# Optimization experiments

Measured on AMD Instinct MI355X. Metric: run time of the kernel, lower is better.

The kernel has to match this reference:

```python
import jax, jax.numpy as jnp
import numpy as np

NUM_HEADS = 16
HIDDEN = 1024
HEADSIZE = HIDDEN // NUM_HEADS


def setup_inputs() -> dict:
    key = jax.random.key(0)
    ks = jax.random.split(key, 9)
    B, S, H = 4, 2048, HIDDEN
    s = 1.0 / np.sqrt(H)
    return {
        "x": jax.random.normal(ks[0], (B, S, H), dtype=jnp.float32),
        "Wq": jax.random.normal(ks[1], (H, H), dtype=jnp.float32) * s,
        "bq": jax.random.normal(ks[2], (H,), dtype=jnp.float32) * s,
        "Wk": jax.random.normal(ks[3], (H, H), dtype=jnp.float32) * s,
        "bk": jax.random.normal(ks[4], (H,), dtype=jnp.float32) * s,
        "Wv": jax.random.normal(ks[5], (H, H), dtype=jnp.float32) * s,
        "bv": jax.random.normal(ks[6], (H,), dtype=jnp.float32) * s,
        "Wo": jax.random.normal(ks[7], (H, H), dtype=jnp.float32) * s,
        "bo": jax.random.normal(ks[8], (H,), dtype=jnp.float32) * s,
    }


def reference(x, Wq, bq, Wk, bk, Wv, bv, Wo, bo):
    B, S, H = x.shape
    nh, hs = NUM_HEADS, HEADSIZE

    def split_heads(y):  # (B,S,H) -> (B,nh,S,hs)
        return y.reshape(B, S, nh, hs).transpose(0, 2, 1, 3)

    q = split_heads(x @ Wq.T + bq)
    k = split_heads(x @ Wk.T + bk)
    v = split_heads(x @ Wv.T + bv)

    scores = jnp.einsum("bhqd,bhkd->bhqk", q, k) / jnp.sqrt(jnp.float32(hs))
    # causal mask: q_ind < k_ind gets -1e9 (matches torch.where(mask, -1e9, scores))
    q_ind = jnp.arange(S)[:, None]
    k_ind = jnp.arange(S)[None, :]
    scores = jnp.where(q_ind < k_ind, jnp.float32(-1e9), scores)
    attn = jax.nn.softmax(scores, axis=-1)
    out = jnp.einsum("bhqk,bhkd->bhqd", attn, v)  # (B,nh,S,hs)
    out = out.transpose(0, 2, 1, 3).reshape(B, S, H)
    return out @ Wo.T + bo
```

## Files before the change

### kernel.cpp

```cpp
#include <hip/hip_runtime.h>

#define NH 16
#define HS 64
#define HID 1024
#define SEQ 2048
#define BB 4
#define MR (BB*SEQ)
#define KD 1024
#define QSCALE 0.18033688f

typedef __bf16 bf16;
typedef __attribute__((ext_vector_type(8))) __bf16 bf16x8;
typedef __attribute__((ext_vector_type(4))) __bf16 bf16x4;
typedef __attribute__((ext_vector_type(4))) float f32x4;
typedef __attribute__((ext_vector_type(16))) float f32x16;
typedef __attribute__((ext_vector_type(4))) float f4;
typedef __attribute__((ext_vector_type(2))) unsigned uintx2;

typedef __attribute__((address_space(3))) unsigned int as3u;
typedef __attribute__((address_space(1))) unsigned int as1u;

__device__ __forceinline__ void gl_lds16(const void* g, void* l) {
  __builtin_amdgcn_global_load_lds((const as1u*)g, (as3u*)l, 16, 0, 0);
}

__device__ __forceinline__ f32x4 mfma16(bf16x8 a, bf16x8 b, f32x4 c) {
  return __builtin_amdgcn_mfma_f32_16x16x32_bf16(a, b, c, 0, 0, 0);
}

__device__ __forceinline__ f32x16 mfma32(bf16x8 a, bf16x8 b, f32x16 c) {
  return __builtin_amdgcn_mfma_f32_32x32x16_bf16(a, b, c, 0, 0, 0);
}

__device__ __forceinline__ uintx2 plswap(unsigned a, unsigned b) {
#if __has_builtin(__builtin_amdgcn_permlane32_swap)
  return __builtin_amdgcn_permlane32_swap(a, b, false, false);
#else
  asm volatile("v_permlane32_swap_b32 %0, %1" : "+&v"(a), "+v"(b));
  uintx2 r; r[0] = a; r[1] = b; return r;
#endif
}

__device__ __forceinline__ float xmax32(float x) {
  uintx2 r = plswap(__float_as_uint(x), __float_as_uint(x));
  return fmaxf(__uint_as_float(r[0]), __uint_as_float(r[1]));
}
__device__ __forceinline__ float xadd32(float x) {
  uintx2 r = plswap(__float_as_uint(x), __float_as_uint(x));
  return __uint_as_float(r[0]) + __uint_as_float(r[1]);
}

__device__ __forceinline__ unsigned cvtpk(float lo, float hi) {
  unsigned r;
  asm("v_cvt_pk_bf16_f32 %0, %1, %2" : "=v"(r) : "v"(lo), "v"(hi));
  return r;
}

__global__ __launch_bounds__(256) void k_cvt(const float* __restrict__ in,
                                             bf16* __restrict__ out, int n4) {
  int i = blockIdx.x * 256 + threadIdx.x;
  if (i >= n4) return;
  f4 v = reinterpret_cast<const f4*>(in)[i];
  bf16x4 h;
  h[0] = (bf16)v[0]; h[1] = (bf16)v[1]; h[2] = (bf16)v[2]; h[3] = (bf16)v[3];
  reinterpret_cast<bf16x4*>(out)[i] = h;
}

__global__ __launch_bounds__(256) void k_cvt4(const float* __restrict__ w0, const float* __restrict__ w1,
                                              const float* __restrict__ w2, const float* __restrict__ w3,
                                              bf16* __restrict__ o0, bf16* __restrict__ o1,
                                              bf16* __restrict__ o2, bf16* __restrict__ o3, int n4) {
  int i = blockIdx.x * 256 + threadIdx.x;
  if (i >= n4) return;
  const float* in = (blockIdx.y == 0) ? w0 : (blockIdx.y == 1) ? w1 : (blockIdx.y == 2) ? w2 : w3;
  bf16* out = (blockIdx.y == 0) ? o0 : (blockIdx.y == 1) ? o1 : (blockIdx.y == 2) ? o2 : o3;
  f4 v = reinterpret_cast<const f4*>(in)[i];
  bf16x4 h;
  h[0] = (bf16)v[0]; h[1] = (bf16)v[1]; h[2] = (bf16)v[2]; h[3] = (bf16)v[3];
  reinterpret_cast<bf16x4*>(out)[i] = h;
}

__global__ __launch_bounds__(256) void k_gemm_qkv(const bf16* __restrict__ A,
                                                  const bf16* __restrict__ wq, const bf16* __restrict__ wk,
                                                  const bf16* __restrict__ wv,
                                                  const float* __restrict__ bq, const float* __restrict__ bk,
                                                  const float* __restrict__ bv,
                                                  bf16* __restrict__ Qo, bf16* __restrict__ Ko,
                                                  bf16* __restrict__ Vo) {
  __shared__ __align__(16) bf16 As[128*32];
  __shared__ __align__(16) bf16 Bs[128*32];
  const int tid = threadIdx.x;
  const int l = tid & 63, w = tid >> 6;
  const int which = blockIdx.y >> 3;
  const int m0 = blockIdx.x * 128, n0 = (blockIdx.y & 7) * 128;
  const int wr = w >> 1, wc = w & 1;

  const bf16* Bw = (which == 0) ? wq : (which == 1) ? wk : wv;
  const float* bias = (which == 0) ? bq : (which == 1) ? bk : bv;

  f32x4 acc[4][4] = {};

  const int srow = 32*w + (l >> 2);
  const int scol = (l & 3) * 8;
  const bf16* Asrc = A  + (size_t)(m0 + srow) * KD + scol;
  const bf16* Bsrc = Bw + (size_t)(n0 + srow) * KD + scol;
  char* AsBase = (char*)As + (size_t)(w*2) * 1024;
  char* BsBase = (char*)Bs + (size_t)(w*2) * 1024;

  for (int kt = 0; kt < KD; kt += 32) {
    gl_lds16(Asrc + kt,                 AsBase);
    gl_lds16(Asrc + kt + (size_t)16*KD, AsBase + 1024);
    gl_lds16(Bsrc + kt,                 BsBase);
    gl_lds16(Bsrc + kt + (size_t)16*KD, BsBase + 1024);
    __syncthreads();

    bf16x8 af[4], bv_[4];
    const int koff = (l >> 4) * 8;
    #pragma unroll
    for (int mf = 0; mf < 4; mf++)
      af[mf] = *reinterpret_cast<const bf16x8*>(&As[(wr*64 + mf*16 + (l & 15))*32 + koff]);
    #pragma unroll
    for (int nf = 0; nf < 4; nf++)
      bv_[nf] = *reinterpret_cast<const bf16x8*>(&Bs[(wc*64 + nf*16 + (l & 15))*32 + koff]);
    #pragma unroll
    for (int mf = 0; mf < 4; mf++)
      #pragma unroll
      for (int nf = 0; nf < 4; nf++)
        acc[mf][nf] = mfma16(af[mf], bv_[nf], acc[mf][nf]);
    __syncthreads();
  }

  const float scale = (which == 0) ? QSCALE : 1.0f;
  #pragma unroll
  for (int mf = 0; mf < 4; mf++) {
    #pragma unroll
    for (int nf = 0; nf < 4; nf++) {
      const int n = n0 + wc*64 + nf*16 + (l & 15);
      const float bn = bias[n];
      #pragma unroll
      for (int j = 0; j < 4; j++) {
        const int m = m0 + wr*64 + mf*16 + (l >> 4)*4 + j;
        const float v = (acc[mf][nf][j] + bn) * scale;
        if (which == 2) {
          Vo[(((size_t)(m >> 11) * NH + (n >> 6)) * HS + (n & 63)) * SEQ + (m & (SEQ-1))] = (bf16)v;
        } else {
          bf16* dst = (which == 0) ? Qo : Ko;
          dst[(((size_t)(m >> 11) * NH + (n >> 6)) * SEQ + (m & (SEQ-1))) * HS + (n & 63)] = (bf16)v;
        }
      }
    }
  }
}

__global__ __launch_bounds__(256) void k_gemm_o(const bf16* __restrict__ A,
                                                const bf16* __restrict__ Bw,
                                                const float* __restrict__ bias,
                                                float* __restrict__ outp) {
  __shared__ __align__(16) bf16 As[128*32];
  __shared__ __align__(16) bf16 Bs[128*32];
  const int tid = threadIdx.x;
  const int l = tid & 63, w = tid >> 6;
  const int m0 = blockIdx.x * 128, n0 = blockIdx.y * 128;
  const int wr = w >> 1, wc = w & 1;

  f32x4 acc[4][4] = {};

  const int srow = 32*w + (l >> 2);
  const int scol = (l & 3) * 8;
  const bf16* Asrc = A  + (size_t)(m0 + srow) * KD + scol;
  const bf16* Bsrc = Bw + (size_t)(n0 + srow) * KD + scol;
  char* AsBase = (char*)As + (size_t)(w*2) * 1024;
  char* BsBase = (char*)Bs + (size_t)(w*2) * 1024;

  for (int kt = 0; kt < KD; kt += 32) {
    gl_lds16(Asrc + kt,                 AsBase);
    gl_lds16(Asrc + kt + (size_t)16*KD, AsBase + 1024);
    gl_lds16(Bsrc + kt,                 BsBase);
    gl_lds16(Bsrc + kt + (size_t)16*KD, BsBase + 1024);
    __syncthreads();

    bf16x8 af[4], bv_[4];
    const int koff = (l >> 4) * 8;
    #pragma unroll
    for (int mf = 0; mf < 4; mf++)
      af[mf] = *reinterpret_cast<const bf16x8*>(&As[(wr*64 + mf*16 + (l & 15))*32 + koff]);
    #pragma unroll
    for (int nf = 0; nf < 4; nf++)
      bv_[nf] = *reinterpret_cast<const bf16x8*>(&Bs[(wc*64 + nf*16 + (l & 15))*32 + koff]);
    #pragma unroll
    for (int mf = 0; mf < 4; mf++)
      #pragma unroll
      for (int nf = 0; nf < 4; nf++)
        acc[mf][nf] = mfma16(af[mf], bv_[nf], acc[mf][nf]);
    __syncthreads();
  }

  #pragma unroll
  for (int mf = 0; mf < 4; mf++) {
    #pragma unroll
    for (int nf = 0; nf < 4; nf++) {
      const int n = n0 + wc*64 + nf*16 + (l & 15);
      const float bn = bias[n];
      #pragma unroll
      for (int j = 0; j < 4; j++) {
        const int m = m0 + wr*64 + mf*16 + (l >> 4)*4 + j;
        outp[(size_t)m * HID + n] = acc[mf][nf][j] + bn;
      }
    }
  }
}

__global__ __launch_bounds__(256, 2) void k_attn(const bf16* __restrict__ Q,
                                                 const bf16* __restrict__ K,
                                                 const bf16* __restrict__ Vt,
                                                 bf16* __restrict__ Aout) {
  const int bh = blockIdx.y;
  const int bx = blockIdx.x;
  const int tid = threadIdx.x, l = tid & 63, w = tid >> 6;
  const int hi = l >> 5;

  __shared__ __align__(16) bf16 Qs[128*64];
  __shared__ __align__(16) bf16 Ks[2][64*64];
  __shared__ __align__(16) bf16 Vs[2][64*64];

  const bf16* Qg = Q  + (size_t)bh * SEQ * HS;
  const bf16* Kg = K  + (size_t)bh * SEQ * HS;
  const bf16* Vg = Vt + (size_t)bh * HS * SEQ;

  const int bb = bh >> 4, hh = bh & 15;
  const int sr  = tid >> 3;
  const int swz = ((tid & 7) ^ (sr & 7)) * 8;

  for (int pass = 0; pass < 2; ++pass) {
    const int p_ = pass ? (15 - bx) : bx;
    const int q0 = p_ * 128;
    const int nt = 2 * p_ + 2;

    __syncthreads();

    #pragma unroll
    for (int i = 0; i < 4; i++)
      gl_lds16(Qg + (size_t)(q0 + 32*i + sr) * HS + swz, (char*)Qs + i*4096 + w*1024);
    #pragma unroll
    for (int i = 0; i < 2; i++) {
      gl_lds16(Kg + (size_t)(32*i + sr) * HS + swz,  (char*)Ks[0] + i*4096 + w*1024);
      gl_lds16(Vg + (size_t)(32*i + sr) * SEQ + swz, (char*)Vs[0] + i*4096 + w*1024);
    }
    __syncthreads();

    bf16x8 qf[4];
    {
      const int qrow = w*32 + (l & 31);
      #pragma unroll
      for (int m = 0; m < 4; m++) {
        const int cc = 2*m + hi;
        qf[m] = *(const bf16x8*)((const char*)Qs + qrow*128 + ((cc ^ (qrow & 7))*16));
      }
    }

    float m_r = -1e30f, l_r = 0.f;
    f32x16 o[2] = {};
    const int qmax = q0 + w*32 + 31;
    const int qg   = q0 + w*32 + (l & 31);

    int cur = 0;
    for (int kt = 0; kt < nt; ++kt) {
      const int k0 = kt * 64;

      if (kt + 1 < nt) {
        const int k1 = k0 + 64;
        #pragma unroll
        for (int i = 0; i < 2; i++) {
          gl_lds16(Kg + (size_t)(k1 + 32*i + sr) * HS + swz,  (char*)Ks[cur^1] + i*4096 + w*1024);
          gl_lds16(Vg + (size_t)(32*i + sr) * SEQ + k1 + swz, (char*)Vs[cur^1] + i*4096 + w*1024);
        }
      }

      if (k0 <= qmax) {
        f32x16 p[2] = {};
        #pragma unroll
        for (int b = 0; b < 2; b++) {
          #pragma unroll
          for (int m = 0; m < 4; m++) {
            const int row = 32*b + (l & 31);
            const int cc = 2*m + hi;
            bf16x8 kf = *(const bf16x8*)((const char*)Ks[cur] + row*128 + ((cc ^ (row & 7))*16));
            p[b] = mfma32(kf, qf[m], p[b]);
          }
        }

        if (k0 + 63 > q0 + w*32) {
          #pragma unroll
          for (int b = 0; b < 2; b++)
            #pragma unroll
            for (int r = 0; r < 16; r++) {
              const int kg = k0 + 32*b + (r & 3) + 8*(r >> 2) + 4*hi;
              if (kg > qg) p[b][r] = -1e30f;
            }
        }

        float rloc = -1e30f;
        #pragma unroll
        for (int b = 0; b < 2; b++)
          #pragma unroll
          for (int r = 0; r < 16; r++) rloc = fmaxf(rloc, p[b][r]);
        const float rmax = xmax32(rloc);

        if (__any(rmax > m_r + 8.0f)) {
          const float mn = fmaxf(m_r, rmax);
          const float alpha = __builtin_amdgcn_exp2f(m_r - mn);
          m_r = mn;
          l_r *= alpha;
          #pragma unroll
          for (int r = 0; r < 16; r++) {
            const float ar = __shfl(alpha, (r & 3) + 8*(r >> 2) + 4*hi);
            o[0][r] *= ar; o[1][r] *= ar;
          }
        }

        float sloc = 0.f;
        #pragma unroll
        for (int b = 0; b < 2; b++)
          #pragma unroll
          for (int r = 0; r < 16; r++) {
            const float e = __builtin_amdgcn_exp2f(p[b][r] - m_r);
            p[b][r] = e;
            sloc += e;
          }
        l_r += xadd32(sloc);

        bf16x8 pa[4];
        #pragma unroll
        for (int c = 0; c < 4; c++) {
          const int b = c >> 1, R = (c & 1) * 8;
          unsigned w01 = cvtpk(p[b][R+0], p[b][R+1]);
          unsigned w23 = cvtpk(p[b][R+2], p[b][R+3]);
          unsigned w89 = cvtpk(p[b][R+4], p[b][R+5]);
          unsigned wab = cvtpk(p[b][R+6], p[b][R+7]);
          uintx2 s1 = plswap(w01, w89);
          uintx2 s2 = plswap(w23, wab);
          union { unsigned u[4]; bf16x8 v; } uu;
          uu.u[0] = s1[0]; uu.u[1] = s2[0]; uu.u[2] = s1[1]; uu.u[3] = s2[1];
          pa[c] = uu.v;
        }

        #pragma unroll
        for (int d = 0; d < 2; d++) {
          #pragma unroll
          for (int c = 0; c < 4; c++) {
            const int row = 32*d + (l & 31);
            const int cc = 2*c + hi;
            bf16x8 vf = *(const bf16x8*)((const char*)Vs[cur] + row*128 + ((cc ^ (row & 7))*16));
            o[d] = mfma32(pa[c], vf, o[d]);
          }
        }
      }

      __syncthreads();
      cur ^= 1;
    }

    const float inv = 1.0f / l_r;
    #pragma unroll
    for (int r = 0; r < 16; r++) {
      const int qr = (r & 3) + 8*(r >> 2) + 4*hi;
      const float ir = __shfl(inv, qr);
      const int q = q0 + w*32 + qr;
      #pragma unroll
      for (int d = 0; d < 2; d++)
        Aout[(size_t)(bb*SEQ + q)*HID + hh*HS + d*32 + (l & 31)] = (bf16)(o[d][r] * ir);
    }
  }
}

extern "C" void kernel_launch(void* const* d_in, const int* in_sizes, int n_in,
                              void* d_out, int out_size, void* d_ws, size_t ws_size,
                              hipStream_t stream) {
  const float* x  = (const float*)d_in[0];
  const float* Wq = (const float*)d_in[1];
  const float* bq = (const float*)d_in[2];
  const float* Wk = (const float*)d_in[3];
  const float* bk = (const float*)d_in[4];
  const float* Wv = (const float*)d_in[5];
  const float* bv = (const float*)d_in[6];
  const float* Wo = (const float*)d_in[7];
  const float* bo = (const float*)d_in[8];

  char* ws = (char*)d_ws;
  const size_t MB = 1024 * 1024;
  bf16* xb  = (bf16*)(ws);
  bf16* wqb = (bf16*)(ws + 16*MB);
  bf16* wkb = (bf16*)(ws + 18*MB);
  bf16* wvb = (bf16*)(ws + 20*MB);
  bf16* wob = (bf16*)(ws + 22*MB);
  bf16* Qb  = (bf16*)(ws + 24*MB);
  bf16* Kb  = (bf16*)(ws + 40*MB);
  bf16* Vb  = (bf16*)(ws + 56*MB);
  bf16* Ab  = xb;

  k_cvt<<<MR*HID/4/256, 256, 0, stream>>>(x, xb, MR*HID/4);
  k_cvt4<<<dim3(HID*KD/4/256, 4), 256, 0, stream>>>(Wq, Wk, Wv, Wo, wqb, wkb, wvb, wob, HID*KD/4);

  k_gemm_qkv<<<dim3(MR/128, 24), 256, 0, stream>>>(xb, wqb, wkb, wvb, bq, bk, bv, Qb, Kb, Vb);

  k_attn<<<dim3(8, BB*NH), 256, 0, stream>>>(Qb, Kb, Vb, Ab);

  k_gemm_o<<<dim3(MR/128, HID/128), 256, 0, stream>>>(Ab, wob, bo, (float*)d_out);
}
```

Measured before the change: 179.7 us.

## Replace QKV and output GEMMs with triple-buffered 128x256 pipelined template kernel

Merges the QKV and output projection GEMMs into one templated kernel that uses 512 threads, a 128x256 tile, and a three-stage LDS ring. Global-to-LDS loads for two tiles ahead are issued while MFMAs run, using explicit vmcnt/lgkmcnt waits, a single barrier per k-step, and raised wave priority around the MFMA blocks. LDS columns are XOR-swizzled to cut bank conflicts. The aim is to hide global load latency and drop the second barrier per iteration. The cost is higher LDS use (72KB per block), which limits occupancy, and a more fragile hand-written wait-count scheme.

```diff
diff --git a/kernel.cpp b/kernel.cpp
--- a/kernel.cpp
+++ b/kernel.cpp
@@ -7,6 +7,7 @@
 #define BB 4
 #define MR (BB*SEQ)
 #define KD 1024
+#define NT 32
 #define QSCALE 0.18033688f
 
 typedef __bf16 bf16;
@@ -80,131 +81,120 @@
   reinterpret_cast<bf16x4*>(out)[i] = h;
 }
 
-__global__ __launch_bounds__(256) void k_gemm_qkv(const bf16* __restrict__ A,
-                                                  const bf16* __restrict__ wq, const bf16* __restrict__ wk,
-                                                  const bf16* __restrict__ wv,
-                                                  const float* __restrict__ bq, const float* __restrict__ bk,
-                                                  const float* __restrict__ bv,
-                                                  bf16* __restrict__ Qo, bf16* __restrict__ Ko,
-                                                  bf16* __restrict__ Vo) {
-  __shared__ __align__(16) bf16 As[128*32];
-  __shared__ __align__(16) bf16 Bs[128*32];
-  const int tid = threadIdx.x;
-  const int l = tid & 63, w = tid >> 6;
-  const int which = blockIdx.y >> 3;
-  const int m0 = blockIdx.x * 128, n0 = (blockIdx.y & 7) * 128;
-  const int wr = w >> 1, wc = w & 1;
-
-  const bf16* Bw = (which == 0) ? wq : (which == 1) ? wk : wv;
-  const float* bias = (which == 0) ? bq : (which == 1) ? bk : bv;
+template<int MODE>
+__global__ __launch_bounds__(512, 4) void k_gemm_p(const bf16* __restrict__ A,
+                                                   const bf16* __restrict__ w0, const bf16* __restrict__ w1,
+                                                   const bf16* __restrict__ w2,
+                                                   const float* __restrict__ b0, const float* __restrict__ b1,
+                                                   const float* __restrict__ b2p,
+                                                   void* __restrict__ o0, void* __restrict__ o1,
+                                                   void* __restrict__ o2) {
+  __shared__ __align__(16) bf16 As[3][128*32];
+  __shared__ __align__(16) bf16 Bs[3][256*32];
+  const int tid = threadIdx.x, l = tid & 63, w = tid >> 6;
+  const int wr = w >> 2, wc = w & 3;
+  const int m0 = blockIdx.x * 128;
+  const int ny = blockIdx.y;
+  const int which = (MODE == 0) ? (ny >> 2) : 0;
+  const int n0 = (MODE == 0) ? (ny & 3) * 256 : ny * 256;
+  const bf16* Bw = (MODE == 1) ? w0 : (which == 0 ? w0 : which == 1 ? w1 : w2);
+  const float* bias = (MODE == 1) ? b0 : (which == 0 ? b0 : which == 1 ? b1 : b2p);
+
+  const int sra = tid >> 2;
+  const int sca = (tid & 3) ^ ((sra >> 1) & 3);
+  const bf16* Ag = A  + (size_t)(m0 + sra) * KD + sca * 8;
+  const bf16* Bg = Bw + (size_t)(n0 + sra) * KD + sca * 8;
+
+  gl_lds16(Ag,                        (char*)As[0] + w * 1024);
+  gl_lds16(Bg,                        (char*)Bs[0] + w * 1024);
+  gl_lds16(Bg + (size_t)128 * KD,     (char*)Bs[0] + 8192 + w * 1024);
+  gl_lds16(Ag + 32,                   (char*)As[1] + w * 1024);
+  gl_lds16(Bg + 32,                   (char*)Bs[1] + w * 1024);
+  gl_lds16(Bg + (size_t)128 * KD + 32, (char*)Bs[1] + 8192 + w * 1024);
 
   f32x4 acc[4][4] = {};
 
-  const int srow = 32*w + (l >> 2);
-  const int scol = (l & 3) * 8;
-  const bf16* Asrc = A  + (size_t)(m0 + srow) * KD + scol;
-  const bf16* Bsrc = Bw + (size_t)(n0 + srow) * KD + scol;
-  char* AsBase = (char*)As + (size_t)(w*2) * 1024;
-  char* BsBase = (char*)Bs + (size_t)(w*2) * 1024;
-
-  for (int kt = 0; kt < KD; kt += 32) {
-    gl_lds16(Asrc + kt,                 AsBase);
-    gl_lds16(Asrc + kt + (size_t)16*KD, AsBase + 1024);
-    gl_lds16(Bsrc + kt,                 BsBase);
-    gl_lds16(Bsrc + kt + (size_t)16*KD, BsBase + 1024);
-    __syncthreads();
-
-    bf16x8 af[4], bv_[4];
-    const int koff = (l >> 4) * 8;
-    #pragma unroll
-    for (int mf = 0; mf < 4; mf++)
-      af[mf] = *reinterpret_cast<const bf16x8*>(&As[(wr*64 + mf*16 + (l & 15))*32 + koff]);
-    #pragma unroll
-    for (int nf = 0; nf < 4; nf++)
-      bv_[nf] = *reinterpret_cast<const bf16x8*>(&Bs[(wc*64 + nf*16 + (l & 15))*32 + koff]);
-    #pragma unroll
-    for (int mf = 0; mf < 4; mf++)
-      #pragma unroll
-      for (int nf = 0; nf < 4; nf++)
-        acc[mf][nf] = mfma16(af[mf], bv_[nf], acc[mf][nf]);
-    __syncthreads();
+  const int la = l & 15, lg = l >> 4;
+
+  for (int t = 0; t < NT; ++t) {
+    const int bq = t % 3;
+    if (t < NT - 1) { asm volatile("s_waitcnt vmcnt(3)" ::: "memory"); }
+    else            { asm volatile("s_waitcnt vmcnt(0)" ::: "memory"); }
+    __builtin_amdgcn_sched_barrier(0);
+    __builtin_amdgcn_s_barrier();
+    __builtin_amdgcn_sched_barrier(0);
+
+    bf16x8 af[4], bf_[2];
+    #pragma unroll
+    for (int mf = 0; mf < 4; mf++) {
+      const int ra = wr * 64 + mf * 16 + la;
+      const int ca = lg ^ ((ra >> 1) & 3);
+      af[mf] = *(const bf16x8*)((const char*)As[bq] + ra * 64 + ca * 16);
+    }
+    #pragma unroll
+    for (int nf = 0; nf < 2; nf++) {
+      const int rb = wc * 64 + nf * 16 + la;
+      const int cb = lg ^ ((rb >> 1) & 3);
+      bf_[nf] = *(const bf16x8*)((const char*)Bs[bq] + rb * 64 + cb * 16);
+    }
+    const int t2 = t + 2;
+    if (t2 < NT) {
+      const int b2 = t2 % 3;
+      gl_lds16(Ag + t2 * 32, (char*)As[b2] + w * 1024);
+      gl_lds16(Bg + t2 * 32, (char*)Bs[b2] + w * 1024);
+    }
+    asm volatile("s_waitcnt lgkmcnt(0)" ::: "memory");
+    __builtin_amdgcn_sched_barrier(0);
+    __builtin_amdgcn_s_setprio(1);
+    #pragma unroll
+    for (int mf = 0; mf < 4; mf++) {
+      acc[mf][0] = mfma16(af[mf], bf_[0], acc[mf][0]);
+      acc[mf][1] = mfma16(af[mf], bf_[1], acc[mf][1]);
+    }
+    __builtin_amdgcn_s_setprio(0);
+
+    #pragma unroll
+    for (int nf = 0; nf < 2; nf++) {
+      const int rb = wc * 64 + (nf + 2) * 16 + la;
+      const int cb = lg ^ ((rb >> 1) & 3);
+      bf_[nf] = *(const bf16x8*)((const char*)Bs[bq] + rb * 64 + cb * 16);
+    }
+    if (t2 < NT) {
+      const int b2 = t2 % 3;
+      gl_lds16(Bg + (size_t)128 * KD + t2 * 32, (char*)Bs[b2] + 8192 + w * 1024);
+    }
+    asm volatile("s_waitcnt lgkmcnt(0)" ::: "memory");
+    __builtin_amdgcn_sched_barrier(0);
+    __builtin_amdgcn_s_setprio(1);
+    #pragma unroll
+    for (int mf = 0; mf < 4; mf++) {
+      acc[mf][2] = mfma16(af[mf], bf_[0], acc[mf][2]);
+      acc[mf][3] = mfma16(af[mf], bf_[1], acc[mf][3]);
+    }
+    __builtin_amdgcn_s_setprio(0);
   }
 
-  const float scale = (which == 0) ? QSCALE : 1.0f;
+  const float scale = (MODE == 0 && which == 0) ? QSCALE : 1.0f;
   #pragma unroll
   for (int mf = 0; mf < 4; mf++) {
     #pragma unroll
     for (int nf = 0; nf < 4; nf++) {
-      const int n = n0 + wc*64 + nf*16 + (l & 15);
+      const int n = n0 + wc * 64 + nf * 16 + la;
       const float bn = bias[n];
       #pragma unroll
       for (int j = 0; j < 4; j++) {
-        const int m = m0 + wr*64 + mf*16 + (l >> 4)*4 + j;
+        const int m = m0 + wr * 64 + mf * 16 + lg * 4 + j;
         const float v = (acc[mf][nf][j] + bn) * scale;
-        if (which == 2) {
-          Vo[(((size_t)(m >> 11) * NH + (n >> 6)) * HS + (n & 63)) * SEQ + (m & (SEQ-1))] = (bf16)v;
+        if (MODE == 0) {
+          if (which == 2) {
+            ((bf16*)o2)[(((size_t)(m >> 11) * NH + (n >> 6)) * HS + (n & 63)) * SEQ + (m & (SEQ - 1))] = (bf16)v;
+          } else {
+            bf16* dst = (which == 0) ? (bf16*)o0 : (bf16*)o1;
+            dst[(((size_t)(m >> 11) * NH + (n >> 6)) * SEQ + (m & (SEQ - 1))) * HS + (n & 63)] = (bf16)v;
+          }
         } else {
-          bf16* dst = (which == 0) ? Qo : Ko;
-          dst[(((size_t)(m >> 11) * NH + (n >> 6)) * SEQ + (m & (SEQ-1))) * HS + (n & 63)] = (bf16)v;
-        }
-      }
-    }
-  }
-}
-
-__global__ __launch_bounds__(256) void k_gemm_o(const bf16* __restrict__ A,
-                                                const bf16* __restrict__ Bw,
-                                                const float* __restrict__ bias,
-                                                float* __restrict__ outp) {
-  __shared__ __align__(16) bf16 As[128*32];
-  __shared__ __align__(16) bf16 Bs[128*32];
-  const int tid = threadIdx.x;
-  const int l = tid & 63, w = tid >> 6;
-  const int m0 = blockIdx.x * 128, n0 = blockIdx.y * 128;
-  const int wr = w >> 1, wc = w & 1;
-
-  f32x4 acc[4][4] = {};
-
-  const int srow = 32*w + (l >> 2);
-  const int scol = (l & 3) * 8;
-  const bf16* Asrc = A  + (size_t)(m0 + srow) * KD + scol;
-  const bf16* Bsrc = Bw + (size_t)(n0 + srow) * KD + scol;
-  char* AsBase = (char*)As + (size_t)(w*2) * 1024;
-  char* BsBase = (char*)Bs + (size_t)(w*2) * 1024;
-
-  for (int kt = 0; kt < KD; kt += 32) {
-    gl_lds16(Asrc + kt,                 AsBase);
-    gl_lds16(Asrc + kt + (size_t)16*KD, AsBase + 1024);
-    gl_lds16(Bsrc + kt,                 BsBase);
-    gl_lds16(Bsrc + kt + (size_t)16*KD, BsBase + 1024);
-    __syncthreads();
-
-    bf16x8 af[4], bv_[4];
-    const int koff = (l >> 4) * 8;
-    #pragma unroll
-    for (int mf = 0; mf < 4; mf++)
-      af[mf] = *reinterpret_cast<const bf16x8*>(&As[(wr*64 + mf*16 + (l & 15))*32 + koff]);
-    #pragma unroll
-    for (int nf = 0; nf < 4; nf++)
-      bv_[nf] = *reinterpret_cast<const bf16x8*>(&Bs[(wc*64 + nf*16 + (l & 15))*32 + koff]);
-    #pragma unroll
-    for (int mf = 0; mf < 4; mf++)
-      #pragma unroll
-      for (int nf = 0; nf < 4; nf++)
-        acc[mf][nf] = mfma16(af[mf], bv_[nf], acc[mf][nf]);
-    __syncthreads();
-  }
-
-  #pragma unroll
-  for (int mf = 0; mf < 4; mf++) {
-    #pragma unroll
-    for (int nf = 0; nf < 4; nf++) {
-      const int n = n0 + wc*64 + nf*16 + (l & 15);
-      const float bn = bias[n];
-      #pragma unroll
-      for (int j = 0; j < 4; j++) {
-        const int m = m0 + wr*64 + mf*16 + (l >> 4)*4 + j;
-        outp[(size_t)m * HID + n] = acc[mf][nf][j] + bn;
+          ((float*)o0)[(size_t)m * HID + n] = v;
+        }
       }
     }
   }
@@ -401,9 +391,9 @@
   k_cvt<<<MR*HID/4/256, 256, 0, stream>>>(x, xb, MR*HID/4);
   k_cvt4<<<dim3(HID*KD/4/256, 4), 256, 0, stream>>>(Wq, Wk, Wv, Wo, wqb, wkb, wvb, wob, HID*KD/4);
 
-  k_gemm_qkv<<<dim3(MR/128, 24), 256, 0, stream>>>(xb, wqb, wkb, wvb, bq, bk, bv, Qb, Kb, Vb);
+  k_gemm_p<0><<<dim3(MR/128, 12), 512, 0, stream>>>(xb, wqb, wkb, wvb, bq, bk, bv, Qb, Kb, Vb);
 
   k_attn<<<dim3(8, BB*NH), 256, 0, stream>>>(Qb, Kb, Vb, Ab);
 
-  k_gemm_o<<<dim3(MR/128, HID/128), 256, 0, stream>>>(Ab, wob, bo, (float*)d_out);
-}
+  k_gemm_p<1><<<dim3(MR/128, 4), 512, 0, stream>>>(Ab, wob, wob, wob, bo, bo, bo, d_out, d_out, d_out);
+}
```

Measured after the change: 170.7 us. 5.0% less time.
